# Kernel tuning notes

Hardware: AMD Instinct MI355X
Metric: run time of the kernel (lower is better)

Reference implementation:

```python
import jax, jax.numpy as jnp
import numpy as np

N_NODES = 100000
N_EDGES = 3200000
F_X = 24
F_S = 8
H = 64
F_OUT = 32


def setup_inputs() -> dict:
    key = jax.random.key(0)
    ks = jax.random.split(key, 6)
    x = jax.random.normal(ks[0], (N_NODES, F_X), dtype=jnp.float32)
    scalars = jax.random.normal(ks[1], (F_S,), dtype=jnp.float32)
    edge_index = jax.random.randint(ks[2], (2, N_EDGES), 0, N_NODES, dtype=jnp.int64)
    d_in = F_X + F_S
    W1 = jax.random.normal(ks[3], (d_in, H), dtype=jnp.float32) * (1.0 / np.sqrt(d_in))
    b1 = jnp.zeros((H,), dtype=jnp.float32)
    W2 = jax.random.normal(ks[4], (H, F_OUT), dtype=jnp.float32) * (1.0 / np.sqrt(H))
    b2 = jnp.zeros((F_OUT,), dtype=jnp.float32)
    return {"x": x, "scalars": scalars, "edge_index": edge_index,
            "W1": W1, "b1": b1, "W2": W2, "b2": b2}


def reference(x, scalars, edge_index, W1, b1, W2, b2):
    n = x.shape[0]
    # scalars.view(1,-1).expand(N,-1) then cat along feature dim
    s = jnp.broadcast_to(scalars.reshape(1, -1), (n, scalars.shape[-1]))
    h = jnp.concatenate([x, s], axis=1)  # [N, F_X+F_S]
    src, dst = edge_index[0], edge_index[1]
    # per-edge MLP on gathered source features
    m = h[src]                              # [E, d_in] gather
    m = jax.nn.relu(m @ W1 + b1)            # [E, H]
    m = m @ W2 + b2                         # [E, F_OUT]
    # scatter-add aggregation at destination nodes
    out = jax.ops.segment_sum(m, dst, num_segments=n)  # [N, F_OUT]
    return out
```

## Files before the change

kernel.cpp:

```cpp
#include <hip/hip_runtime.h>

#define N_NODES 100000
#define N_EDGES 3200000
#define F_X 24
#define F_S 8
#define D_IN 32
#define H_DIM 64
#define F_OUT 32

#define NPB 256
#define NBKT 391
#define P1_THREADS 1024
#define P1_EPT 16
#define P1_EPB (P1_THREADS * P1_EPT)
#define P1_BLOCKS ((N_EDGES + P1_EPB - 1) / P1_EPB)
#define MLP_BLOCKS ((N_NODES + 255) / 256)
#define P2_THREADS 512
#define OFFS_ROW 392

#define HPB 128
#define BCAP_H 4608

__device__ __forceinline__ unsigned bf16_rne(float f) {
    unsigned u = __float_as_uint(f);
    return (u + 0x7fffu + ((u >> 16) & 1u)) >> 16;
}

__global__ __launch_bounds__(P1_THREADS) void fused_mlp_p1(
    const float* __restrict__ x, const float* __restrict__ scalars,
    const float* __restrict__ W1, const float* __restrict__ b1,
    const float* __restrict__ W2, const float* __restrict__ b2,
    unsigned* __restrict__ y,
    const int* __restrict__ ei,
    unsigned* __restrict__ bbuf,
    int* __restrict__ offs_g)
{
    __shared__ __align__(16) unsigned char smem[68736];
    const int tid = threadIdx.x;

    if (blockIdx.x < P1_BLOCKS) {
        unsigned* sSE  = (unsigned*)smem;
        int* cnt       = (int*)(smem + 65536);
        int* runoff    = (int*)(smem + 67104);
        int* wsum      = (int*)(smem + 68672);

        const int nbase = blockIdx.x * P1_EPB;
        const int nThis = min(P1_EPB, N_EDGES - nbase);

        for (int i = tid; i < NBKT; i += P1_THREADS) cnt[i] = 0;
        __syncthreads();

        unsigned pk[P1_EPT];
        int meta[P1_EPT];
        #pragma unroll
        for (int k = 0; k < P1_EPT; ++k) {
            const int idx = tid + k * P1_THREADS;
            if (idx < nThis) {
                const int e = nbase + idx;
                const int src = ei[e];
                const int dst = ei[N_EDGES + e];
                const int bkt = dst >> 8;
                const int rank = atomicAdd(&cnt[bkt], 1);
                pk[k]   = (unsigned)src | ((unsigned)(dst & 255) << 17);
                meta[k] = bkt | (rank << 9);
            } else {
                meta[k] = -1;
            }
        }
        __syncthreads();

        const int lane = tid & 63, wid = tid >> 6;
        const int cval = (tid < NBKT) ? cnt[tid] : 0;
        int a = cval;
        #pragma unroll
        for (int off = 1; off < 64; off <<= 1) {
            const int u = __shfl_up(a, off, 64);
            if (lane >= off) a += u;
        }
        if (lane == 63) wsum[wid] = a;
        __syncthreads();
        if (tid == 0) {
            int r = 0;
            #pragma unroll
            for (int w = 0; w < 7; ++w) { const int t = wsum[w]; wsum[w] = r; r += t; }
        }
        __syncthreads();
        if (tid <= NBKT) {
            const int bse = wsum[wid] + a - cval;
            runoff[tid] = bse;
            offs_g[blockIdx.x * OFFS_ROW + tid] = bse;
        }
        __syncthreads();

        #pragma unroll
        for (int k = 0; k < P1_EPT; ++k) {
            if (meta[k] >= 0)
                sSE[runoff[meta[k] & 511] + (meta[k] >> 9)] = pk[k];
        }
        __syncthreads();

        const uint4* s4 = (const uint4*)sSE;
        uint4* b4 = (uint4*)(bbuf + (size_t)blockIdx.x * P1_EPB);
        for (int i = tid; i < (nThis >> 2); i += P1_THREADS) b4[i] = s4[i];
    } else {
        float* sW1 = (float*)smem;
        float* sW2 = (float*)(smem + 8192);
        float* sb1 = (float*)(smem + 16384);
        float* sb2 = (float*)(smem + 16640);
        float* ss  = (float*)(smem + 16768);

        for (int i = tid; i < D_IN * H_DIM; i += P1_THREADS) sW1[i] = W1[i];
        for (int i = tid; i < H_DIM * F_OUT; i += P1_THREADS) sW2[i] = W2[i];
        if (tid < H_DIM)  sb1[tid] = b1[tid];
        if (tid < F_OUT)  sb2[tid] = b2[tid];
        if (tid < F_S)    ss[tid]  = scalars[tid];
        __syncthreads();

        const int mb = blockIdx.x - P1_BLOCKS;
        const int v = mb * 256 + (tid >> 2);
        const int c = tid & 3;
        if (v >= N_NODES) return;

        float h[D_IN];
        const float4* xr = reinterpret_cast<const float4*>(x + (size_t)v * F_X);
        #pragma unroll
        for (int i = 0; i < F_X / 4; ++i) {
            float4 t = xr[i];
            h[i * 4 + 0] = t.x; h[i * 4 + 1] = t.y;
            h[i * 4 + 2] = t.z; h[i * 4 + 3] = t.w;
        }
        #pragma unroll
        for (int i = 0; i < F_S; ++i) h[F_X + i] = ss[i];

        float hid[16];
        {
            const float4* bb = reinterpret_cast<const float4*>(sb1 + c * 16);
            #pragma unroll
            for (int q = 0; q < 4; ++q) {
                const float4 t = bb[q];
                hid[q * 4 + 0] = t.x; hid[q * 4 + 1] = t.y;
                hid[q * 4 + 2] = t.z; hid[q * 4 + 3] = t.w;
            }
        }
        #pragma unroll
        for (int k = 0; k < D_IN; ++k) {
            const float hk = h[k];
            const float4* wr = reinterpret_cast<const float4*>(sW1 + k * H_DIM + c * 16);
            #pragma unroll
            for (int q = 0; q < 4; ++q) {
                const float4 t = wr[q];
                hid[q * 4 + 0] = fmaf(hk, t.x, hid[q * 4 + 0]);
                hid[q * 4 + 1] = fmaf(hk, t.y, hid[q * 4 + 1]);
                hid[q * 4 + 2] = fmaf(hk, t.z, hid[q * 4 + 2]);
                hid[q * 4 + 3] = fmaf(hk, t.w, hid[q * 4 + 3]);
            }
        }
        #pragma unroll
        for (int l = 0; l < 16; ++l) hid[l] = fmaxf(hid[l], 0.0f);

        float op[8];
        #pragma unroll
        for (int t = 0; t < 8; ++t) op[t] = 0.0f;

        #pragma unroll
        for (int d = 0; d < 4; ++d) {
            const int cc = c ^ d;
            float ht[16];
            if (d == 0) {
                #pragma unroll
                for (int t = 0; t < 16; ++t) ht[t] = hid[t];
            } else {
                #pragma unroll
                for (int t = 0; t < 16; ++t) ht[t] = __shfl_xor(hid[t], d);
            }
            const int lbase = cc * 16;
            #pragma unroll
            for (int ll = 0; ll < 16; ++ll) {
                const float hl = ht[ll];
                const float4* wr = reinterpret_cast<const float4*>(
                    sW2 + (lbase + ll) * F_OUT + c * 8);
                const float4 t0 = wr[0], t1 = wr[1];
                op[0] = fmaf(hl, t0.x, op[0]);
                op[1] = fmaf(hl, t0.y, op[1]);
                op[2] = fmaf(hl, t0.z, op[2]);
                op[3] = fmaf(hl, t0.w, op[3]);
                op[4] = fmaf(hl, t1.x, op[4]);
                op[5] = fmaf(hl, t1.y, op[5]);
                op[6] = fmaf(hl, t1.z, op[6]);
                op[7] = fmaf(hl, t1.w, op[7]);
            }
        }
        #pragma unroll
        for (int t = 0; t < 8; ++t) op[t] += sb2[c * 8 + t];

        unsigned pk4[4];
        #pragma unroll
        for (int t = 0; t < 4; ++t)
            pk4[t] = bf16_rne(op[2 * t]) | (bf16_rne(op[2 * t + 1]) << 16);
        uint4* yr = reinterpret_cast<uint4*>(y + (size_t)v * 16 + c * 4);
        *yr = make_uint4(pk4[0], pk4[1], pk4[2], pk4[3]);
    }
}

__global__ __launch_bounds__(P2_THREADS) void p2_aggregate(
    const unsigned* __restrict__ bbuf,
    const int* __restrict__ offs_g,
    const unsigned* __restrict__ y,
    float* __restrict__ out)
{
    __shared__ unsigned sS[BCAP_H];
    __shared__ int segsrc[P1_BLOCKS];
    __shared__ int seglen[P1_BLOCKS];
    __shared__ int cnt[HPB];
    __shared__ int cur[HPB];
    __shared__ int cbase[HPB + 1];
    __shared__ int wsumT[3];

    const int tid = threadIdx.x;
    const int bkt = blockIdx.x >> 1;
    const int h   = blockIdx.x & 1;
    const int lane = tid & 63, wid = tid >> 6;

    if (tid < P1_BLOCKS) {
        const int o0 = offs_g[tid * OFFS_ROW + bkt];
        segsrc[tid] = o0;
        seglen[tid] = offs_g[tid * OFFS_ROW + bkt + 1] - o0;
    }
    if (tid < HPB) cnt[tid] = 0;
    __syncthreads();

    for (int i = wid; i < P1_BLOCKS; i += P2_THREADS / 64) {
        const int cI = seglen[i];
        const unsigned* gp = bbuf + (size_t)i * P1_EPB + segsrc[i];
        for (int j = lane; j < cI; j += 64) {
            const int dl = (int)((gp[j] >> 17) & 255u);
            if ((dl >> 7) == h) atomicAdd(&cnt[dl & 127], 1);
        }
    }
    __syncthreads();

    int vcnt = 0, a2 = 0;
    if (tid < HPB) {
        vcnt = cnt[tid];
        a2 = vcnt;
        #pragma unroll
        for (int off = 1; off < 64; off <<= 1) {
            const int u = __shfl_up(a2, off, 64);
            if (lane >= off) a2 += u;
        }
        if (lane == 63) wsumT[tid >> 6] = a2;
    }
    __syncthreads();
    if (tid == 0) {
        int r = 0;
        #pragma unroll
        for (int w = 0; w < 2; ++w) { const int t = wsumT[w]; wsumT[w] = r; r += t; }
        wsumT[2] = r;
    }
    __syncthreads();
    if (tid < HPB) {
        const int bse = wsumT[tid >> 6] + a2 - vcnt;
        cbase[tid] = bse;
        cur[tid]   = bse;
        if (tid == HPB - 1) cbase[HPB] = wsumT[2];
    }
    __syncthreads();

    for (int i = wid; i < P1_BLOCKS; i += P2_THREADS / 64) {
        const int cI = seglen[i];
        const unsigned* gp = bbuf + (size_t)i * P1_EPB + segsrc[i];
        for (int j = lane; j < cI; j += 64) {
            const unsigned w = gp[j];
            const int dl = (int)((w >> 17) & 255u);
            if ((dl >> 7) == h) {
                const int pos = atomicAdd(&cur[dl & 127], 1);
                if (pos < BCAP_H) sS[pos] = w & 0x1FFFFu;
            }
        }
    }
    __syncthreads();

    const int g = tid >> 2;
    const int c = tid & 3;
    int beg = cbase[g];
    int end = cbase[g + 1];
    if (end > BCAP_H) end = BCAP_H;
    if (beg > BCAP_H) beg = BCAP_H;

    float acc[8];
    #pragma unroll
    for (int k = 0; k < 8; ++k) acc[k] = 0.0f;

    int i = beg;
    for (; i + 4 <= end; i += 4) {
        unsigned s[4];
        #pragma unroll
        for (int j = 0; j < 4; ++j) s[j] = sS[i + j];

        uint4 q[4];
        #pragma unroll
        for (int j = 0; j < 4; ++j)
            q[j] = reinterpret_cast<const uint4*>(y + (size_t)s[j] * 16)[c];

        __builtin_amdgcn_sched_barrier(0);

        #pragma unroll
        for (int j = 0; j < 4; ++j) {
            const unsigned qq[4] = {q[j].x, q[j].y, q[j].z, q[j].w};
            #pragma unroll
            for (int k = 0; k < 4; ++k) {
                acc[2 * k + 0] += __uint_as_float(qq[k] << 16);
                acc[2 * k + 1] += __uint_as_float(qq[k] & 0xFFFF0000u);
            }
        }
    }
    for (; i < end; ++i) {
        const uint4 q = reinterpret_cast<const uint4*>(y + (size_t)sS[i] * 16)[c];
        const unsigned qq[4] = {q.x, q.y, q.z, q.w};
        #pragma unroll
        for (int k = 0; k < 4; ++k) {
            acc[2 * k + 0] += __uint_as_float(qq[k] << 16);
            acc[2 * k + 1] += __uint_as_float(qq[k] & 0xFFFF0000u);
        }
    }

    const int v = bkt * NPB + h * HPB + g;
    if (v < N_NODES) {
        float4* op = reinterpret_cast<float4*>(out + (size_t)v * F_OUT + c * 8);
        op[0] = make_float4(acc[0], acc[1], acc[2], acc[3]);
        op[1] = make_float4(acc[4], acc[5], acc[6], acc[7]);
    }
}

extern "C" void kernel_launch(void* const* d_in, const int* in_sizes, int n_in,
                              void* d_out, int out_size, void* d_ws, size_t ws_size,
                              hipStream_t stream) {
    const float* x       = (const float*)d_in[0];
    const float* scalars = (const float*)d_in[1];
    const int*   ei      = (const int*)d_in[2];
    const float* W1      = (const float*)d_in[3];
    const float* b1      = (const float*)d_in[4];
    const float* W2      = (const float*)d_in[5];
    const float* b2      = (const float*)d_in[6];
    float* out = (float*)d_out;

    char* ws = (char*)d_ws;
    unsigned* y      = (unsigned*)ws;
    unsigned* bbuf   = (unsigned*)(ws + 6400000);
    int*      offs_g = (int*)(ws + 19245056);

    fused_mlp_p1<<<P1_BLOCKS + MLP_BLOCKS, P1_THREADS, 0, stream>>>(
        x, scalars, W1, b1, W2, b2, y, ei, bbuf, offs_g);

    p2_aggregate<<<NBKT * 2, P2_THREADS, 0, stream>>>(bbuf, offs_g, y, out);
}
```

Measured before the change: 96.90 us.

## Bucket edges by 128 destinations and split gathers by source half

The first pass now buckets edges into 782 buckets of 128 destinations, so each aggregate block reads only its own edges instead of scanning 256-node buckets twice. Each aggregate block loads its segments into shared memory once through a binary-search compaction, then bins them by destination and by which half of the source range they fall in. The gather then runs in two phases separated by a block barrier, so concurrent blocks tend to touch the same half of y and improve cache locality. The costs are extra shared memory, a per-element binary search and an added barrier.

After: 79.04 us. 1.23x faster.

```diff
diff --git a/kernel.cpp b/kernel.cpp
--- a/kernel.cpp
+++ b/kernel.cpp
@@ -8,18 +8,17 @@
 #define H_DIM 64
 #define F_OUT 32
 
-#define NPB 256
-#define NBKT 391
+#define NBKT2 782
+#define HPB 128
+#define BCAP_H 4608
 #define P1_THREADS 1024
 #define P1_EPT 16
 #define P1_EPB (P1_THREADS * P1_EPT)
 #define P1_BLOCKS ((N_EDGES + P1_EPB - 1) / P1_EPB)
 #define MLP_BLOCKS ((N_NODES + 255) / 256)
 #define P2_THREADS 512
-#define OFFS_ROW 392
-
-#define HPB 128
-#define BCAP_H 4608
+#define OFFS_ROW 783
+#define SRC_SPLIT 50000
 
 __device__ __forceinline__ unsigned bf16_rne(float f) {
     unsigned u = __float_as_uint(f);
@@ -35,19 +34,19 @@
     unsigned* __restrict__ bbuf,
     int* __restrict__ offs_g)
 {
-    __shared__ __align__(16) unsigned char smem[68736];
+    __shared__ __align__(16) unsigned char smem[71928];
     const int tid = threadIdx.x;
 
     if (blockIdx.x < P1_BLOCKS) {
         unsigned* sSE  = (unsigned*)smem;
         int* cnt       = (int*)(smem + 65536);
-        int* runoff    = (int*)(smem + 67104);
-        int* wsum      = (int*)(smem + 68672);
+        int* runoff    = (int*)(smem + 68664);
+        int* wsum      = (int*)(smem + 71796);
 
         const int nbase = blockIdx.x * P1_EPB;
         const int nThis = min(P1_EPB, N_EDGES - nbase);
 
-        for (int i = tid; i < NBKT; i += P1_THREADS) cnt[i] = 0;
+        for (int i = tid; i < NBKT2; i += P1_THREADS) cnt[i] = 0;
         __syncthreads();
 
         unsigned pk[P1_EPT];
@@ -59,10 +58,10 @@
                 const int e = nbase + idx;
                 const int src = ei[e];
                 const int dst = ei[N_EDGES + e];
-                const int bkt = dst >> 8;
+                const int bkt = dst >> 7;
                 const int rank = atomicAdd(&cnt[bkt], 1);
-                pk[k]   = (unsigned)src | ((unsigned)(dst & 255) << 17);
-                meta[k] = bkt | (rank << 9);
+                pk[k]   = (unsigned)src | ((unsigned)(dst & 127) << 17);
+                meta[k] = bkt | (rank << 10);
             } else {
                 meta[k] = -1;
             }
@@ -70,7 +69,7 @@
         __syncthreads();
 
         const int lane = tid & 63, wid = tid >> 6;
-        const int cval = (tid < NBKT) ? cnt[tid] : 0;
+        const int cval = (tid < NBKT2) ? cnt[tid] : 0;
         int a = cval;
         #pragma unroll
         for (int off = 1; off < 64; off <<= 1) {
@@ -82,10 +81,10 @@
         if (tid == 0) {
             int r = 0;
             #pragma unroll
-            for (int w = 0; w < 7; ++w) { const int t = wsum[w]; wsum[w] = r; r += t; }
-        }
-        __syncthreads();
-        if (tid <= NBKT) {
+            for (int w = 0; w < 16; ++w) { const int t = wsum[w]; wsum[w] = r; r += t; }
+        }
+        __syncthreads();
+        if (tid <= NBKT2) {
             const int bse = wsum[wid] + a - cval;
             runoff[tid] = bse;
             offs_g[blockIdx.x * OFFS_ROW + tid] = bse;
@@ -95,7 +94,7 @@
         #pragma unroll
         for (int k = 0; k < P1_EPT; ++k) {
             if (meta[k] >= 0)
-                sSE[runoff[meta[k] & 511] + (meta[k] >> 9)] = pk[k];
+                sSE[runoff[meta[k] & 1023] + (meta[k] >> 10)] = pk[k];
         }
         __syncthreads();
 
@@ -208,39 +207,64 @@
     const unsigned* __restrict__ y,
     float* __restrict__ out)
 {
+    __shared__ unsigned sE[BCAP_H];
     __shared__ unsigned sS[BCAP_H];
     __shared__ int segsrc[P1_BLOCKS];
-    __shared__ int seglen[P1_BLOCKS];
-    __shared__ int cnt[HPB];
-    __shared__ int cur[HPB];
-    __shared__ int cbase[HPB + 1];
-    __shared__ int wsumT[3];
+    __shared__ int segoff[P1_BLOCKS + 1];
+    __shared__ int cnt[2 * HPB];
+    __shared__ int cbase[2 * HPB + 1];
+    __shared__ int wtmp[16];
 
     const int tid = threadIdx.x;
-    const int bkt = blockIdx.x >> 1;
-    const int h   = blockIdx.x & 1;
+    const int bkt = blockIdx.x;
     const int lane = tid & 63, wid = tid >> 6;
 
+    int slen = 0;
     if (tid < P1_BLOCKS) {
         const int o0 = offs_g[tid * OFFS_ROW + bkt];
+        slen = offs_g[tid * OFFS_ROW + bkt + 1] - o0;
         segsrc[tid] = o0;
-        seglen[tid] = offs_g[tid * OFFS_ROW + bkt + 1] - o0;
-    }
-    if (tid < HPB) cnt[tid] = 0;
-    __syncthreads();
-
-    for (int i = wid; i < P1_BLOCKS; i += P2_THREADS / 64) {
-        const int cI = seglen[i];
-        const unsigned* gp = bbuf + (size_t)i * P1_EPB + segsrc[i];
-        for (int j = lane; j < cI; j += 64) {
-            const int dl = (int)((gp[j] >> 17) & 255u);
-            if ((dl >> 7) == h) atomicAdd(&cnt[dl & 127], 1);
-        }
+    }
+    int sa = slen;
+    #pragma unroll
+    for (int off = 1; off < 64; off <<= 1) {
+        const int u = __shfl_up(sa, off, 64);
+        if (lane >= off) sa += u;
+    }
+    if (lane == 63 && wid < 4) wtmp[wid] = sa;
+    if (tid < 2 * HPB) cnt[tid] = 0;
+    __syncthreads();
+    if (tid == 0) {
+        int r = 0;
+        #pragma unroll
+        for (int w = 0; w < 4; ++w) { const int t = wtmp[w]; wtmp[w] = r; r += t; }
+        segoff[P1_BLOCKS] = (r < BCAP_H) ? r : BCAP_H;
+    }
+    __syncthreads();
+    if (tid < P1_BLOCKS) segoff[tid] = wtmp[wid] + sa - slen;
+    __syncthreads();
+
+    const int nE = segoff[P1_BLOCKS];
+
+    for (int i = tid; i < nE; i += P2_THREADS) {
+        int lo = 0, hi = P1_BLOCKS - 1;
+        while (lo < hi) {
+            const int mid = (lo + hi + 1) >> 1;
+            if (segoff[mid] <= i) lo = mid; else hi = mid - 1;
+        }
+        sE[i] = bbuf[(size_t)lo * P1_EPB + segsrc[lo] + (i - segoff[lo])];
+    }
+    __syncthreads();
+
+    for (int i = tid; i < nE; i += P2_THREADS) {
+        const unsigned w = sE[i];
+        const int bin = (int)((w >> 17) & 127u) * 2 + ((w & 0x1FFFFu) >= SRC_SPLIT);
+        atomicAdd(&cnt[bin], 1);
     }
     __syncthreads();
 
     int vcnt = 0, a2 = 0;
-    if (tid < HPB) {
+    if (tid < 2 * HPB) {
         vcnt = cnt[tid];
         a2 = vcnt;
         #pragma unroll
@@ -248,83 +272,80 @@
             const int u = __shfl_up(a2, off, 64);
             if (lane >= off) a2 += u;
         }
-        if (lane == 63) wsumT[tid >> 6] = a2;
+        if (lane == 63) wtmp[8 + wid] = a2;
     }
     __syncthreads();
     if (tid == 0) {
         int r = 0;
         #pragma unroll
-        for (int w = 0; w < 2; ++w) { const int t = wsumT[w]; wsumT[w] = r; r += t; }
-        wsumT[2] = r;
-    }
-    __syncthreads();
-    if (tid < HPB) {
-        const int bse = wsumT[tid >> 6] + a2 - vcnt;
-        cbase[tid] = bse;
-        cur[tid]   = bse;
-        if (tid == HPB - 1) cbase[HPB] = wsumT[2];
-    }
-    __syncthreads();
-
-    for (int i = wid; i < P1_BLOCKS; i += P2_THREADS / 64) {
-        const int cI = seglen[i];
-        const unsigned* gp = bbuf + (size_t)i * P1_EPB + segsrc[i];
-        for (int j = lane; j < cI; j += 64) {
-            const unsigned w = gp[j];
-            const int dl = (int)((w >> 17) & 255u);
-            if ((dl >> 7) == h) {
-                const int pos = atomicAdd(&cur[dl & 127], 1);
-                if (pos < BCAP_H) sS[pos] = w & 0x1FFFFu;
-            }
-        }
+        for (int w = 0; w < 4; ++w) { const int t = wtmp[8 + w]; wtmp[8 + w] = r; r += t; }
+        cbase[2 * HPB] = r;
+    }
+    __syncthreads();
+    if (tid < 2 * HPB) cbase[tid] = wtmp[8 + wid] + a2 - vcnt;
+    __syncthreads();
+    if (tid < 2 * HPB) cnt[tid] = cbase[tid];
+    __syncthreads();
+
+    for (int i = tid; i < nE; i += P2_THREADS) {
+        const unsigned w = sE[i];
+        const unsigned src = w & 0x1FFFFu;
+        const int bin = (int)((w >> 17) & 127u) * 2 + (src >= SRC_SPLIT);
+        const int pos = atomicAdd(&cnt[bin], 1);
+        if (pos < BCAP_H) sS[pos] = src;
     }
     __syncthreads();
 
     const int g = tid >> 2;
     const int c = tid & 3;
-    int beg = cbase[g];
-    int end = cbase[g + 1];
-    if (end > BCAP_H) end = BCAP_H;
-    if (beg > BCAP_H) beg = BCAP_H;
 
     float acc[8];
     #pragma unroll
     for (int k = 0; k < 8; ++k) acc[k] = 0.0f;
 
-    int i = beg;
-    for (; i + 4 <= end; i += 4) {
-        unsigned s[4];
-        #pragma unroll
-        for (int j = 0; j < 4; ++j) s[j] = sS[i + j];
-
-        uint4 q[4];
-        #pragma unroll
-        for (int j = 0; j < 4; ++j)
-            q[j] = reinterpret_cast<const uint4*>(y + (size_t)s[j] * 16)[c];
-
-        __builtin_amdgcn_sched_barrier(0);
-
-        #pragma unroll
-        for (int j = 0; j < 4; ++j) {
-            const unsigned qq[4] = {q[j].x, q[j].y, q[j].z, q[j].w};
+    #pragma unroll
+    for (int ph = 0; ph < 2; ++ph) {
+        int beg = cbase[2 * g + ph];
+        int end = cbase[2 * g + ph + 1];
+        if (beg > BCAP_H) beg = BCAP_H;
+        if (end > BCAP_H) end = BCAP_H;
+
+        int i = beg;
+        for (; i + 4 <= end; i += 4) {
+            unsigned s[4];
+            #pragma unroll
+            for (int j = 0; j < 4; ++j) s[j] = sS[i + j];
+
+            uint4 q[4];
+            #pragma unroll
+            for (int j = 0; j < 4; ++j)
+                q[j] = reinterpret_cast<const uint4*>(y + (size_t)s[j] * 16)[c];
+
+            __builtin_amdgcn_sched_barrier(0);
+
+            #pragma unroll
+            for (int j = 0; j < 4; ++j) {
+                const unsigned qq[4] = {q[j].x, q[j].y, q[j].z, q[j].w};
+                #pragma unroll
+                for (int k = 0; k < 4; ++k) {
+                    acc[2 * k + 0] += __uint_as_float(qq[k] << 16);
+                    acc[2 * k + 1] += __uint_as_float(qq[k] & 0xFFFF0000u);
+                }
+            }
+        }
+        for (; i < end; ++i) {
+            const uint4 q = reinterpret_cast<const uint4*>(y + (size_t)sS[i] * 16)[c];
+            const unsigned qq[4] = {q.x, q.y, q.z, q.w};
             #pragma unroll
             for (int k = 0; k < 4; ++k) {
                 acc[2 * k + 0] += __uint_as_float(qq[k] << 16);
                 acc[2 * k + 1] += __uint_as_float(qq[k] & 0xFFFF0000u);
             }
         }
-    }
-    for (; i < end; ++i) {
-        const uint4 q = reinterpret_cast<const uint4*>(y + (size_t)sS[i] * 16)[c];
-        const unsigned qq[4] = {q.x, q.y, q.z, q.w};
-        #pragma unroll
-        for (int k = 0; k < 4; ++k) {
-            acc[2 * k + 0] += __uint_as_float(qq[k] << 16);
-            acc[2 * k + 1] += __uint_as_float(qq[k] & 0xFFFF0000u);
-        }
-    }
-
-    const int v = bkt * NPB + h * HPB + g;
+        if (ph == 0) __syncthreads();
+    }
+
+    const int v = bkt * HPB + g;
     if (v < N_NODES) {
         float4* op = reinterpret_cast<float4*>(out + (size_t)v * F_OUT + c * 8);
         op[0] = make_float4(acc[0], acc[1], acc[2], acc[3]);
@@ -352,5 +373,5 @@
     fused_mlp_p1<<<P1_BLOCKS + MLP_BLOCKS, P1_THREADS, 0, stream>>>(
         x, scalars, W1, b1, W2, b2, y, ei, bbuf, offs_g);
 
-    p2_aggregate<<<NBKT * 2, P2_THREADS, 0, stream>>>(bbuf, offs_g, y, out);
+    p2_aggregate<<<NBKT2, P2_THREADS, 0, stream>>>(bbuf, offs_g, y, out);
 }
```
